# Kernel optimization log

Hardware: AMD Instinct MI355X
Metric: run time of the kernel (lower is better)

## Reference

```python
import jax, jax.numpy as jnp
import numpy as np

N_QUBITS = 4
N_LAYERS = 3
H_IMG = 512

# ---------- 4-qubit statevector simulator, batched over P patches ----------

def _apply_1q(psi, U, w):
    # shared 2x2 gate U on wire w; psi: (P,2,2,2,2)
    psi = jnp.moveaxis(psi, 1 + w, -1)
    psi = jnp.einsum('ij,...j->...i', U, psi)
    return jnp.moveaxis(psi, -1, 1 + w)

def _apply_1q_batched(psi, U, w):
    # per-patch gate U: (P,2,2)
    psi = jnp.moveaxis(psi, 1 + w, -1)
    psi = jnp.einsum('pij,p...j->p...i', U, psi)
    return jnp.moveaxis(psi, -1, 1 + w)

def _apply_cnot(psi, c, t):
    psi = jnp.moveaxis(psi, (1 + c, 1 + t), (-2, -1))
    top = psi[..., 0:1, :]
    bot = psi[..., 1:2, ::-1]  # X on target when control=1
    psi = jnp.concatenate([top, bot], axis=-2)
    return jnp.moveaxis(psi, (-2, -1), (1 + c, 1 + t))

def _rx(theta):
    # AngleEmbedding default rotation='X'; theta: (P,) -> (P,2,2)
    h = theta * 0.5
    c = jnp.cos(h).astype(jnp.complex64)
    s = (-1j * jnp.sin(h)).astype(jnp.complex64)
    return jnp.stack([jnp.stack([c, s], -1), jnp.stack([s, c], -1)], -2)

def _rot(phi, theta, omega):
    # PennyLane Rot = RZ(omega) RY(theta) RZ(phi)
    c = jnp.cos(theta * 0.5)
    s = jnp.sin(theta * 0.5)
    em = jnp.exp(-0.5j * (phi + omega))
    ep = jnp.exp(0.5j * (phi + omega))
    fm = jnp.exp(0.5j * (phi - omega))
    fp = jnp.exp(-0.5j * (phi - omega))
    row0 = jnp.stack([em * c, -fm * s])
    row1 = jnp.stack([fp * s, ep * c])
    return jnp.stack([row0, row1]).astype(jnp.complex64)

def _qsim(inputs, weights):
    # inputs: (P,4) angles; weights: (3,4,3) Rot params -> (P,4) PauliZ expvals
    P = inputs.shape[0]
    psi = jnp.zeros((P, 2, 2, 2, 2), jnp.complex64).at[:, 0, 0, 0, 0].set(1.0)
    for w in range(N_QUBITS):
        psi = _apply_1q_batched(psi, _rx(inputs[:, w]), w)
    for l in range(N_LAYERS):
        for w in range(N_QUBITS):
            psi = _apply_1q(psi, _rot(weights[l, w, 0], weights[l, w, 1], weights[l, w, 2]), w)
        r = (l % (N_QUBITS - 1)) + 1  # StronglyEntanglingLayers default ranges
        for w in range(N_QUBITS):
            psi = _apply_cnot(psi, w, (w + r) % N_QUBITS)
    probs = psi.real ** 2 + psi.imag ** 2  # (P,2,2,2,2)
    ez = []
    for w in range(N_QUBITS):
        axes = tuple(a for a in range(1, 5) if a != 1 + w)
        p = probs.sum(axes)  # (P,2)
        ez.append(p[:, 0] - p[:, 1])
    return jnp.stack(ez, -1)  # (P,4)

def _qconv(x, q_weights):
    img = x[0, 0]  # (H,W)
    a = img[:-1, :-1]; b = img[:-1, 1:]; c = img[1:, :-1]; d = img[1:, 1:]
    Hm, Wm = a.shape
    patches = jnp.stack([a, b, c, d], -1).reshape(-1, 4)  # row-major 2x2 flatten
    ez = _qsim(patches, q_weights)  # (P,4)
    return ez.reshape(Hm, Wm, 4).transpose(2, 0, 1)[None]  # (1,4,Hm,Wm)

# ---------- classical layers ----------

def _conv(x, w, b):
    y = jax.lax.conv_general_dilated(x, w, (1, 1), 'VALID',
                                     dimension_numbers=('NCHW', 'OIHW', 'NCHW'))
    return y + b[None, :, None, None]

def _maxpool2(x):
    return jax.lax.reduce_window(x, -jnp.inf, jax.lax.max,
                                 (1, 1, 2, 2), (1, 1, 2, 2), 'VALID')

def _adaptive_max(x, out):
    H, W = x.shape[-2], x.shape[-1]
    rows = []
    for i in range(out):
        si, ei = (i * H) // out, -(-((i + 1) * H) // out)
        cols = []
        for j in range(out):
            sj, ej = (j * W) // out, -(-((j + 1) * W) // out)
            cols.append(x[..., si:ei, sj:ej].max((-2, -1)))
        rows.append(jnp.stack(cols, -1))
    return jnp.stack(rows, -2)


def setup_inputs() -> dict:
    key = jax.random.key(0)
    ks = jax.random.split(key, 10)
    x = jax.random.normal(ks[0], (1, 1, H_IMG, H_IMG), jnp.float32)
    q_weights = jax.random.uniform(ks[1], (N_LAYERS, N_QUBITS, 3), jnp.float32,
                                   0.0, 2.0 * np.pi)
    conv2_w = jax.random.normal(ks[2], (20, 4, 5, 5), jnp.float32) * 0.05
    conv2_b = jax.random.normal(ks[3], (20,), jnp.float32) * 0.05
    conv3_w = jax.random.normal(ks[4], (40, 20, 3, 3), jnp.float32) * 0.05
    conv3_b = jax.random.normal(ks[5], (40,), jnp.float32) * 0.05
    fc1_w = jax.random.normal(ks[6], (64, 640), jnp.float32) * 0.05
    fc1_b = jax.random.normal(ks[7], (64,), jnp.float32) * 0.05
    fc2_w = jax.random.normal(ks[8], (10, 64), jnp.float32) * 0.05
    fc2_b = jax.random.normal(ks[9], (10,), jnp.float32) * 0.05
    return {'x': x, 'q_weights': q_weights,
            'conv2_w': conv2_w, 'conv2_b': conv2_b,
            'conv3_w': conv3_w, 'conv3_b': conv3_b,
            'fc1_w': fc1_w, 'fc1_b': fc1_b,
            'fc2_w': fc2_w, 'fc2_b': fc2_b}


def reference(x, q_weights, conv2_w, conv2_b, conv3_w, conv3_b,
              fc1_w, fc1_b, fc2_w, fc2_b):
    h = _maxpool2(jax.nn.sigmoid(_qconv(x, q_weights)))        # (1,4,255,255)
    h = _maxpool2(jax.nn.relu(_conv(h, conv2_w, conv2_b)))      # (1,20,125,125)
    h = _adaptive_max(jax.nn.relu(_conv(h, conv3_w, conv3_b)), 4)  # (1,40,4,4)
    h = h.reshape(-1, 640)
    h = jax.nn.relu(h @ fc1_w.T + fc1_b)
    return h @ fc2_w.T + fc2_b  # (1,10)
```

## Files before the change

kernel.cpp:

```cpp
#include <hip/hip_runtime.h>
#include <math.h>

#define IMG 512
#define QO  255
#define QP  256
#define C2H 125
#define C2S 128
#define C3H 123

template<int M_>
__device__ inline void rot_regs(float2* a, float2 U00, float2 U01, float2 U10, float2 U11) {
    #pragma unroll
    for (int s = 0; s < 16; ++s) {
        if (!(s & M_)) {
            float2 a0 = a[s], a1 = a[s | M_];
            a[s]      = make_float2(U00.x*a0.x - U00.y*a0.y + U01.x*a1.x - U01.y*a1.y,
                                    U00.x*a0.y + U00.y*a0.x + U01.x*a1.y + U01.y*a1.x);
            a[s | M_] = make_float2(U10.x*a0.x - U10.y*a0.y + U11.x*a1.x - U11.y*a1.y,
                                    U10.x*a0.y + U10.y*a0.x + U11.x*a1.y + U11.y*a1.x);
        }
    }
}
template<int MC, int MT>
__device__ inline void cnot_regs(float2* a) {
    #pragma unroll
    for (int s = 0; s < 16; ++s) {
        if ((s & MC) && !(s & MT)) {
            float2 t = a[s]; a[s] = a[s | MT]; a[s | MT] = t;
        }
    }
}
__device__ inline void rot_gate_params(float phi, float th, float om,
                                       float2& U00, float2& U01, float2& U10, float2& U11) {
    float ch, sh, ca, sa, cb, sb;
    __sincosf(0.5f * th, &sh, &ch);
    __sincosf(0.5f * (phi + om), &sa, &ca);
    __sincosf(0.5f * (phi - om), &sb, &cb);
    U00 = make_float2( ca*ch, -sa*ch);
    U01 = make_float2(-cb*sh, -sb*sh);
    U10 = make_float2( cb*sh, -sb*sh);
    U11 = make_float2( ca*ch,  sa*ch);
}

__global__ __launch_bounds__(256) void qconv_pool(const float* __restrict__ img,
                                                  const float* __restrict__ qw,
                                                  float* __restrict__ out) {
    __shared__ float2 Ms[256];
    int tid = threadIdx.x;

    if (tid < 16) {
        float2 a[16];
        #pragma unroll
        for (int s = 0; s < 16; ++s) a[s] = make_float2(s == tid ? 1.f : 0.f, 0.f);
        float2 U00, U01, U10, U11;
#define ROTG(L, W) rot_gate_params(qw[((L)*4+(W))*3+0], qw[((L)*4+(W))*3+1], qw[((L)*4+(W))*3+2], U00,U01,U10,U11); \
                   rot_regs<(1 << (3-(W)))>(a, U00, U01, U10, U11);
        ROTG(0,0) ROTG(0,1) ROTG(0,2) ROTG(0,3)
        cnot_regs<8,4>(a); cnot_regs<4,2>(a); cnot_regs<2,1>(a); cnot_regs<1,8>(a);
        ROTG(1,0) ROTG(1,1) ROTG(1,2) ROTG(1,3)
        cnot_regs<8,2>(a); cnot_regs<4,1>(a); cnot_regs<2,8>(a); cnot_regs<1,4>(a);
        ROTG(2,0) ROTG(2,1) ROTG(2,2) ROTG(2,3)
        cnot_regs<8,1>(a); cnot_regs<4,8>(a); cnot_regs<2,4>(a); cnot_regs<1,2>(a);
#undef ROTG
        int pc4 = __popc(tid) & 3;
        #pragma unroll
        for (int row = 0; row < 16; ++row) {
            float2 v = a[row], o;
            if      (pc4 == 0) o = v;
            else if (pc4 == 1) o = make_float2( v.y, -v.x);
            else if (pc4 == 2) o = make_float2(-v.x, -v.y);
            else               o = make_float2(-v.y,  v.x);
            Ms[row * 16 + tid] = o;
        }
    }
    __syncthreads();

    int gid = blockIdx.x * 256 + tid;
    int pid = gid >> 1, p = gid & 1;
    if (pid >= QO * QO) return;
    int i = pid / QO, j = pid - i * QO;
    int r0 = 2 * i + p, c0 = 2 * j;

    float cs[2][3], sn[2][3];
    #pragma unroll
    for (int rr = 0; rr < 2; ++rr)
        #pragma unroll
        for (int cc = 0; cc < 3; ++cc) {
            float v = img[(r0 + rr) * IMG + c0 + cc];
            __sincosf(0.5f * v, &sn[rr][cc], &cs[rr][cc]);
        }

    float mx0 = -1e30f, mx1 = -1e30f, mx2 = -1e30f, mx3 = -1e30f;

    #pragma unroll
    for (int pc = 0; pc < 2; ++pc) {
        float c0v = cs[0][pc],   s0 = sn[0][pc];
        float c1v = cs[0][pc+1], s1 = sn[0][pc+1];
        float c2v = cs[1][pc],   s2 = sn[1][pc];
        float c3v = cs[1][pc+1], s3 = sn[1][pc+1];
        float t01[4] = {c0v*c1v, c0v*s1, s0*c1v, s0*s1};
        float t23[4] = {c2v*c3v, c2v*s3, s2*c3v, s2*s3};
        float a[16];
        #pragma unroll
        for (int k = 0; k < 16; ++k) a[k] = t01[k >> 2] * t23[k & 3];

        float e0 = 0.f, e1 = 0.f, e2 = 0.f, e3 = 0.f;
        #pragma unroll 4
        for (int rw = 0; rw < 16; ++rw) {
            float re = 0.f, im = 0.f;
            #pragma unroll
            for (int k = 0; k < 16; ++k) {
                float2 m = Ms[rw * 16 + k];
                re = fmaf(m.x, a[k], re);
                im = fmaf(m.y, a[k], im);
            }
            float pp = fmaf(re, re, im * im);
            e0 += (rw & 8) ? -pp : pp;
            e1 += (rw & 4) ? -pp : pp;
            e2 += (rw & 2) ? -pp : pp;
            e3 += (rw & 1) ? -pp : pp;
        }
        mx0 = fmaxf(mx0, e0);
        mx1 = fmaxf(mx1, e1);
        mx2 = fmaxf(mx2, e2);
        mx3 = fmaxf(mx3, e3);
    }

    mx0 = fmaxf(mx0, __shfl_xor(mx0, 1, 64));
    mx1 = fmaxf(mx1, __shfl_xor(mx1, 1, 64));
    mx2 = fmaxf(mx2, __shfl_xor(mx2, 1, 64));
    mx3 = fmaxf(mx3, __shfl_xor(mx3, 1, 64));

    if (p == 0) {
        int o = i * QP + j;
        out[0 * QP * QP + o] = 1.f / (1.f + __expf(-mx0));
        out[1 * QP * QP + o] = 1.f / (1.f + __expf(-mx1));
        out[2 * QP * QP + o] = 1.f / (1.f + __expf(-mx2));
        out[3 * QP * QP + o] = 1.f / (1.f + __expf(-mx3));
    }
}

__global__ __launch_bounds__(256) void conv2_pool(const float* __restrict__ in,
                                                  const float* __restrict__ w,
                                                  const float* __restrict__ b,
                                                  float* __restrict__ out,
                                                  float* __restrict__ am) {
    if (blockIdx.x == 0 && blockIdx.y == 0) {
        for (int e = threadIdx.x; e < 640; e += 256) am[e] = 0.f;
    }
    int oc = blockIdx.y;
    int sp = blockIdx.x * 256 + threadIdx.x;
    if (sp >= C2H * C2H) return;
    int i = sp / C2H, j = sp - i * C2H;
    const float* wb = w + oc * 100;

    float a00 = 0.f, a01 = 0.f, a10 = 0.f, a11 = 0.f;
    #pragma unroll
    for (int ic = 0; ic < 4; ++ic) {
        const float* ip = in + ic * QP * QP + (2 * i) * QP + 2 * j;
        float win[6][6];
        #pragma unroll
        for (int y = 0; y < 6; ++y) {
            #pragma unroll
            for (int h = 0; h < 3; ++h) {
                float2 v = *(const float2*)(ip + y * QP + 2 * h);
                win[y][2*h]   = v.x;
                win[y][2*h+1] = v.y;
            }
        }
        #pragma unroll
        for (int ky = 0; ky < 5; ++ky) {
            #pragma unroll
            for (int kx = 0; kx < 5; ++kx) {
                float wv = wb[ic * 25 + ky * 5 + kx];
                a00 = fmaf(win[ky][kx],     wv, a00);
                a01 = fmaf(win[ky][kx+1],   wv, a01);
                a10 = fmaf(win[ky+1][kx],   wv, a10);
                a11 = fmaf(win[ky+1][kx+1], wv, a11);
            }
        }
    }
    float m = fmaxf(fmaxf(a00, a01), fmaxf(a10, a11));
    out[oc * C2H * C2S + i * C2S + j] = fmaxf(m + b[oc], 0.f);
}

__global__ __launch_bounds__(256) void conv3_amax(const float* __restrict__ in,
                                                  const float* __restrict__ w,
                                                  const float* __restrict__ b,
                                                  int* __restrict__ am) {
    __shared__ int bm[64];
    int og = blockIdx.y, oc0 = og * 4;
    if (threadIdx.x < 64) bm[threadIdx.x] = 0;
    __syncthreads();

    int sp = blockIdx.x * 256 + threadIdx.x;
    if (sp < C3H * C3H) {
        int y = sp / C3H, x = sp - y * C3H;
        const float* wb = w + oc0 * 180;

        float acc0 = 0.f, acc1 = 0.f, acc2 = 0.f, acc3 = 0.f;
        #pragma unroll
        for (int ic = 0; ic < 20; ++ic) {
            const float* ip = in + ic * C2H * C2S + y * C2S + x;
            float v[3][3];
            #pragma unroll
            for (int ky = 0; ky < 3; ++ky)
                #pragma unroll
                for (int kx = 0; kx < 3; ++kx)
                    v[ky][kx] = ip[ky * C2S + kx];
            #pragma unroll
            for (int kk = 0; kk < 9; ++kk) {
                float iv = v[kk / 3][kk % 3];
                acc0 = fmaf(iv, wb[      ic * 9 + kk], acc0);
                acc1 = fmaf(iv, wb[180 + ic * 9 + kk], acc1);
                acc2 = fmaf(iv, wb[360 + ic * 9 + kk], acc2);
                acc3 = fmaf(iv, wb[540 + ic * 9 + kk], acc3);
            }
        }
        acc0 = fmaxf(acc0 + b[oc0 + 0], 0.f);
        acc1 = fmaxf(acc1 + b[oc0 + 1], 0.f);
        acc2 = fmaxf(acc2 + b[oc0 + 2], 0.f);
        acc3 = fmaxf(acc3 + b[oc0 + 3], 0.f);

        const int bs[4] = {0, 30, 61, 92};
        const int be[4] = {31, 62, 93, 123};
        #pragma unroll
        for (int yb = 0; yb < 4; ++yb) {
            if (y >= bs[yb] && y < be[yb]) {
                #pragma unroll
                for (int xb = 0; xb < 4; ++xb) {
                    if (x >= bs[xb] && x < be[xb]) {
                        int bin = yb * 4 + xb;
                        atomicMax(&bm[0 * 16 + bin], __float_as_int(acc0));
                        atomicMax(&bm[1 * 16 + bin], __float_as_int(acc1));
                        atomicMax(&bm[2 * 16 + bin], __float_as_int(acc2));
                        atomicMax(&bm[3 * 16 + bin], __float_as_int(acc3));
                    }
                }
            }
        }
    }
    __syncthreads();
    if (threadIdx.x < 64) {
        int v = bm[threadIdx.x];
        if (v != 0)
            atomicMax(&am[(oc0 + (threadIdx.x >> 4)) * 16 + (threadIdx.x & 15)], v);
    }
}

__global__ void fc_k(const float* __restrict__ h, const float* __restrict__ w1,
                     const float* __restrict__ b1, const float* __restrict__ w2,
                     const float* __restrict__ b2, float* __restrict__ out) {
    __shared__ float hh[640];
    __shared__ float h1[64];
    int t = threadIdx.x;
    for (int e = t; e < 640; e += 256) hh[e] = h[e];
    __syncthreads();

    int r = t >> 2, q = t & 3;
    const float4* wr = (const float4*)(w1 + r * 640 + q * 160);
    const float*  hp = hh + q * 160;
    float acc = 0.f;
    #pragma unroll 4
    for (int n = 0; n < 40; ++n) {
        float4 wv = wr[n];
        acc = fmaf(wv.x, hp[n*4+0], acc);
        acc = fmaf(wv.y, hp[n*4+1], acc);
        acc = fmaf(wv.z, hp[n*4+2], acc);
        acc = fmaf(wv.w, hp[n*4+3], acc);
    }
    acc += __shfl_xor(acc, 1, 64);
    acc += __shfl_xor(acc, 2, 64);
    if (q == 0) h1[r] = fmaxf(acc + b1[r], 0.f);
    __syncthreads();

    if (t < 10) {
        float o = b2[t];
        #pragma unroll 8
        for (int n = 0; n < 64; ++n) o = fmaf(h1[n], w2[t * 64 + n], o);
        out[t] = o;
    }
}

extern "C" void kernel_launch(void* const* d_in, const int* in_sizes, int n_in,
                              void* d_out, int out_size, void* d_ws, size_t ws_size,
                              hipStream_t stream) {
    const float* x   = (const float*)d_in[0];
    const float* qw  = (const float*)d_in[1];
    const float* c2w = (const float*)d_in[2];
    const float* c2b = (const float*)d_in[3];
    const float* c3w = (const float*)d_in[4];
    const float* c3b = (const float*)d_in[5];
    const float* f1w = (const float*)d_in[6];
    const float* f1b = (const float*)d_in[7];
    const float* f2w = (const float*)d_in[8];
    const float* f2b = (const float*)d_in[9];
    float* out = (float*)d_out;

    float* wsf   = (float*)d_ws;
    float* qout  = wsf;
    float* c2out = qout + 4 * QP * QP;
    float* am    = c2out + 20 * C2H * C2S;

    qconv_pool<<<(2 * QO * QO + 255) / 256, 256, 0, stream>>>(x, qw, qout);
    conv2_pool<<<dim3((C2H * C2H + 255) / 256, 20), 256, 0, stream>>>(qout, c2w, c2b, c2out, am);
    conv3_amax<<<dim3((C3H * C3H + 255) / 256, 10), 256, 0, stream>>>(c2out, c3w, c3b, (int*)am);
    fc_k<<<1, 256, 0, stream>>>(am, f1w, f1b, f2w, f2b, out);
}
```

Baseline: 142.3 us.

## Precompute symmetric quadratic-form tensors for quantum conv and stage conv weights in LDS

Because the input state is a real product state, the quantum expectation values become a quadratic form. The qconv kernel now builds a 10x10 symmetric Gram-like tensor G4 once per block and evaluates each patch with 100 FMAs per output. This replaces the 16x16 complex matvec per patch. Each thread now handles both pooled rows and shares the middle image row, so the launch uses half as many blocks. Conv2 and conv3 load their weights into shared memory, with conv3 packing them as float4, instead of reading them from global memory per FMA. The cost is extra per-block setup work and two additional syncthreads.

```diff
diff --git a/kernel.cpp b/kernel.cpp
--- a/kernel.cpp
+++ b/kernel.cpp
@@ -42,10 +42,14 @@
     U11 = make_float2( ca*ch,  sa*ch);
 }
 
+__device__ __constant__ int UP1[10] = {0,0,0,0,1,1,1,2,2,3};
+__device__ __constant__ int UP2[10] = {0,1,2,3,1,2,3,2,3,3};
+
 __global__ __launch_bounds__(256) void qconv_pool(const float* __restrict__ img,
                                                   const float* __restrict__ qw,
                                                   float* __restrict__ out) {
     __shared__ float2 Ms[256];
+    __shared__ float4 G4[100];
     int tid = threadIdx.x;
 
     if (tid < 16) {
@@ -75,69 +79,94 @@
     }
     __syncthreads();
 
+    if (tid < 100) {
+        int al = tid / 10, be = tid - 10 * (tid / 10);
+        int u = UP1[al], up = UP2[al], v = UP1[be], vp = UP2[be];
+        float s0 = 0.f, s1 = 0.f, s2 = 0.f, s3 = 0.f;
+        for (int ci = 0; ci < 2; ++ci) {
+            if (ci == 1 && u == up) break;
+            int a1 = ci ? up : u, a2 = ci ? u : up;
+            for (int cj = 0; cj < 2; ++cj) {
+                if (cj == 1 && v == vp) break;
+                int b1 = cj ? vp : v, b2 = cj ? v : vp;
+                int k = a1 * 4 + b1, kp = a2 * 4 + b2;
+                #pragma unroll
+                for (int r = 0; r < 16; ++r) {
+                    float2 m1 = Ms[r * 16 + k], m2 = Ms[r * 16 + kp];
+                    float p = m1.x * m2.x + m1.y * m2.y;
+                    s0 += (r & 8) ? -p : p;
+                    s1 += (r & 4) ? -p : p;
+                    s2 += (r & 2) ? -p : p;
+                    s3 += (r & 1) ? -p : p;
+                }
+            }
+        }
+        G4[tid] = make_float4(s0, s1, s2, s3);
+    }
+    __syncthreads();
+
     int gid = blockIdx.x * 256 + tid;
-    int pid = gid >> 1, p = gid & 1;
-    if (pid >= QO * QO) return;
-    int i = pid / QO, j = pid - i * QO;
-    int r0 = 2 * i + p, c0 = 2 * j;
-
-    float cs[2][3], sn[2][3];
-    #pragma unroll
-    for (int rr = 0; rr < 2; ++rr)
+    if (gid >= QO * QO) return;
+    int i = gid / QO, j = gid - i * QO;
+    int r0 = 2 * i, c0 = 2 * j;
+
+    float cs[3][3], sn[3][3];
+    #pragma unroll
+    for (int rr = 0; rr < 3; ++rr)
         #pragma unroll
         for (int cc = 0; cc < 3; ++cc) {
             float v = img[(r0 + rr) * IMG + c0 + cc];
             __sincosf(0.5f * v, &sn[rr][cc], &cs[rr][cc]);
         }
 
+    float tv[3][2][4];
+    #pragma unroll
+    for (int rr = 0; rr < 3; ++rr)
+        #pragma unroll
+        for (int pc = 0; pc < 2; ++pc) {
+            tv[rr][pc][0] = cs[rr][pc] * cs[rr][pc+1];
+            tv[rr][pc][1] = cs[rr][pc] * sn[rr][pc+1];
+            tv[rr][pc][2] = sn[rr][pc] * cs[rr][pc+1];
+            tv[rr][pc][3] = sn[rr][pc] * sn[rr][pc+1];
+        }
+
     float mx0 = -1e30f, mx1 = -1e30f, mx2 = -1e30f, mx3 = -1e30f;
 
     #pragma unroll
-    for (int pc = 0; pc < 2; ++pc) {
-        float c0v = cs[0][pc],   s0 = sn[0][pc];
-        float c1v = cs[0][pc+1], s1 = sn[0][pc+1];
-        float c2v = cs[1][pc],   s2 = sn[1][pc];
-        float c3v = cs[1][pc+1], s3 = sn[1][pc+1];
-        float t01[4] = {c0v*c1v, c0v*s1, s0*c1v, s0*s1};
-        float t23[4] = {c2v*c3v, c2v*s3, s2*c3v, s2*s3};
-        float a[16];
-        #pragma unroll
-        for (int k = 0; k < 16; ++k) a[k] = t01[k >> 2] * t23[k & 3];
-
-        float e0 = 0.f, e1 = 0.f, e2 = 0.f, e3 = 0.f;
-        #pragma unroll 4
-        for (int rw = 0; rw < 16; ++rw) {
-            float re = 0.f, im = 0.f;
-            #pragma unroll
-            for (int k = 0; k < 16; ++k) {
-                float2 m = Ms[rw * 16 + k];
-                re = fmaf(m.x, a[k], re);
-                im = fmaf(m.y, a[k], im);
-            }
-            float pp = fmaf(re, re, im * im);
-            e0 += (rw & 8) ? -pp : pp;
-            e1 += (rw & 4) ? -pp : pp;
-            e2 += (rw & 2) ? -pp : pp;
-            e3 += (rw & 1) ? -pp : pp;
-        }
-        mx0 = fmaxf(mx0, e0);
-        mx1 = fmaxf(mx1, e1);
-        mx2 = fmaxf(mx2, e2);
-        mx3 = fmaxf(mx3, e3);
-    }
-
-    mx0 = fmaxf(mx0, __shfl_xor(mx0, 1, 64));
-    mx1 = fmaxf(mx1, __shfl_xor(mx1, 1, 64));
-    mx2 = fmaxf(mx2, __shfl_xor(mx2, 1, 64));
-    mx3 = fmaxf(mx3, __shfl_xor(mx3, 1, 64));
-
-    if (p == 0) {
-        int o = i * QP + j;
-        out[0 * QP * QP + o] = 1.f / (1.f + __expf(-mx0));
-        out[1 * QP * QP + o] = 1.f / (1.f + __expf(-mx1));
-        out[2 * QP * QP + o] = 1.f / (1.f + __expf(-mx2));
-        out[3 * QP * QP + o] = 1.f / (1.f + __expf(-mx3));
-    }
+    for (int pr = 0; pr < 2; ++pr) {
+        #pragma unroll
+        for (int pc = 0; pc < 2; ++pc) {
+            float q23[10];
+            #pragma unroll
+            for (int be = 0; be < 10; ++be)
+                q23[be] = tv[pr+1][pc][UP1[be]] * tv[pr+1][pc][UP2[be]];
+
+            float e0 = 0.f, e1 = 0.f, e2 = 0.f, e3 = 0.f;
+            #pragma unroll
+            for (int al = 0; al < 10; ++al) {
+                float pa = tv[pr][pc][UP1[al]] * tv[pr][pc][UP2[al]];
+                #pragma unroll
+                for (int be = 0; be < 10; ++be) {
+                    float4 g = G4[al * 10 + be];
+                    float pq = pa * q23[be];
+                    e0 = fmaf(g.x, pq, e0);
+                    e1 = fmaf(g.y, pq, e1);
+                    e2 = fmaf(g.z, pq, e2);
+                    e3 = fmaf(g.w, pq, e3);
+                }
+            }
+            mx0 = fmaxf(mx0, e0);
+            mx1 = fmaxf(mx1, e1);
+            mx2 = fmaxf(mx2, e2);
+            mx3 = fmaxf(mx3, e3);
+        }
+    }
+
+    int o = i * QP + j;
+    out[0 * QP * QP + o] = 1.f / (1.f + __expf(-mx0));
+    out[1 * QP * QP + o] = 1.f / (1.f + __expf(-mx1));
+    out[2 * QP * QP + o] = 1.f / (1.f + __expf(-mx2));
+    out[3 * QP * QP + o] = 1.f / (1.f + __expf(-mx3));
 }
 
 __global__ __launch_bounds__(256) void conv2_pool(const float* __restrict__ in,
@@ -145,14 +174,19 @@
                                                   const float* __restrict__ b,
                                                   float* __restrict__ out,
                                                   float* __restrict__ am) {
-    if (blockIdx.x == 0 && blockIdx.y == 0) {
+    __shared__ float W[100];
+    __shared__ float Bv;
+    int oc = blockIdx.y;
+    if (threadIdx.x < 100) W[threadIdx.x] = w[oc * 100 + threadIdx.x];
+    if (threadIdx.x == 0) Bv = b[oc];
+    if (blockIdx.x == 0 && oc == 0) {
         for (int e = threadIdx.x; e < 640; e += 256) am[e] = 0.f;
     }
-    int oc = blockIdx.y;
+    __syncthreads();
+
     int sp = blockIdx.x * 256 + threadIdx.x;
     if (sp >= C2H * C2H) return;
     int i = sp / C2H, j = sp - i * C2H;
-    const float* wb = w + oc * 100;
 
     float a00 = 0.f, a01 = 0.f, a10 = 0.f, a11 = 0.f;
     #pragma unroll
@@ -172,7 +206,7 @@
         for (int ky = 0; ky < 5; ++ky) {
             #pragma unroll
             for (int kx = 0; kx < 5; ++kx) {
-                float wv = wb[ic * 25 + ky * 5 + kx];
+                float wv = W[ic * 25 + ky * 5 + kx];
                 a00 = fmaf(win[ky][kx],     wv, a00);
                 a01 = fmaf(win[ky][kx+1],   wv, a01);
                 a10 = fmaf(win[ky+1][kx],   wv, a10);
@@ -181,22 +215,27 @@
         }
     }
     float m = fmaxf(fmaxf(a00, a01), fmaxf(a10, a11));
-    out[oc * C2H * C2S + i * C2S + j] = fmaxf(m + b[oc], 0.f);
+    out[oc * C2H * C2S + i * C2S + j] = fmaxf(m + Bv, 0.f);
 }
 
 __global__ __launch_bounds__(256) void conv3_amax(const float* __restrict__ in,
                                                   const float* __restrict__ w,
                                                   const float* __restrict__ b,
                                                   int* __restrict__ am) {
+    __shared__ float4 W4[180];
     __shared__ int bm[64];
     int og = blockIdx.y, oc0 = og * 4;
+    if (threadIdx.x < 180) {
+        int rr = threadIdx.x;
+        const float* wb = w + oc0 * 180 + rr;
+        W4[rr] = make_float4(wb[0], wb[180], wb[360], wb[540]);
+    }
     if (threadIdx.x < 64) bm[threadIdx.x] = 0;
     __syncthreads();
 
     int sp = blockIdx.x * 256 + threadIdx.x;
     if (sp < C3H * C3H) {
         int y = sp / C3H, x = sp - y * C3H;
-        const float* wb = w + oc0 * 180;
 
         float acc0 = 0.f, acc1 = 0.f, acc2 = 0.f, acc3 = 0.f;
         #pragma unroll
@@ -210,11 +249,12 @@
                     v[ky][kx] = ip[ky * C2S + kx];
             #pragma unroll
             for (int kk = 0; kk < 9; ++kk) {
+                float4 wv = W4[ic * 9 + kk];
                 float iv = v[kk / 3][kk % 3];
-                acc0 = fmaf(iv, wb[      ic * 9 + kk], acc0);
-                acc1 = fmaf(iv, wb[180 + ic * 9 + kk], acc1);
-                acc2 = fmaf(iv, wb[360 + ic * 9 + kk], acc2);
-                acc3 = fmaf(iv, wb[540 + ic * 9 + kk], acc3);
+                acc0 = fmaf(iv, wv.x, acc0);
+                acc1 = fmaf(iv, wv.y, acc1);
+                acc2 = fmaf(iv, wv.z, acc2);
+                acc3 = fmaf(iv, wv.w, acc3);
             }
         }
         acc0 = fmaxf(acc0 + b[oc0 + 0], 0.f);
@@ -302,7 +342,7 @@
     float* c2out = qout + 4 * QP * QP;
     float* am    = c2out + 20 * C2H * C2S;
 
-    qconv_pool<<<(2 * QO * QO + 255) / 256, 256, 0, stream>>>(x, qw, qout);
+    qconv_pool<<<(QO * QO + 255) / 256, 256, 0, stream>>>(x, qw, qout);
     conv2_pool<<<dim3((C2H * C2H + 255) / 256, 20), 256, 0, stream>>>(qout, c2w, c2b, c2out, am);
     conv3_amax<<<dim3((C3H * C3H + 255) / 256, 10), 256, 0, stream>>>(c2out, c3w, c3b, (int*)am);
     fc_k<<<1, 256, 0, stream>>>(am, f1w, f1b, f2w, f2b, out);
```

Result: faster. 134.5 us (-5.5%).
